# Kernel optimization log

Hardware: AMD Instinct MI355X
Metric: run time of the kernel (lower is better)

## Reference

```python
import jax, jax.numpy as jnp
import numpy as np

EPS = 1e-5


def _ln(t):
    # Custom LayerNorm from the source: unbiased variance (torch.var default),
    # gamma=ones, beta=zeros (plain tensors, never trained) -> plain normalize.
    m = t.mean(axis=-1, keepdims=True)
    v = t.var(axis=-1, keepdims=True, ddof=1)
    return (t - m) / jnp.sqrt(v + EPS)


def setup_inputs() -> dict:
    key = jax.random.key(0)
    B, T, C, H = 4, 2048, 1024, 16
    hs = C // H
    ks = jax.random.split(key, 10)
    s_in = (1.0 / C) ** 0.5   # nn.Linear default init scale (approx, uniform->normal ok for ref)
    s_ff = (1.0 / (4 * C)) ** 0.5
    return {
        "x": jax.random.normal(ks[0], (B, T, C), jnp.float32),
        "Wq": jax.random.normal(ks[1], (H, C, hs), jnp.float32) * s_in,
        "Wk": jax.random.normal(ks[2], (H, C, hs), jnp.float32) * s_in,
        "Wv": jax.random.normal(ks[3], (H, C, hs), jnp.float32) * s_in,
        "Wo": jax.random.normal(ks[4], (C, C), jnp.float32) * s_in,
        "bo": jnp.zeros((C,), jnp.float32),
        "W1": jax.random.normal(ks[5], (C, 4 * C), jnp.float32) * s_in,
        "b1": jnp.zeros((4 * C,), jnp.float32),
        "W2": jax.random.normal(ks[6], (4 * C, C), jnp.float32) * s_ff,
        "b2": jnp.zeros((C,), jnp.float32),
    }


def reference(x, Wq, Wk, Wv, Wo, bo, W1, b1, W2, b2):
    B, T, C = x.shape
    H, _, hs = Wq.shape
    # per-head projections (equivalent to the Python loop over Head modules)
    q = jnp.einsum('btc,hcd->bhtd', x, Wq)
    k = jnp.einsum('btc,hcd->bhtd', x, Wk)
    v = jnp.einsum('btc,hcd->bhtd', x, Wv)
    scores = jnp.einsum('bhtd,bhsd->bhts', q, k) * (hs ** -0.5)
    causal = jnp.tril(jnp.ones((T, T), dtype=bool))
    scores = jnp.where(causal, scores, jnp.float32(-jnp.inf))
    w = jax.nn.softmax(scores, axis=-1)          # dropout is identity in eval
    o = jnp.einsum('bhts,bhsd->bhtd', w, v)
    o = o.transpose(0, 2, 1, 3).reshape(B, T, C)  # concat heads
    attn = o @ Wo + bo
    x1 = x + _ln(attn)
    ff = jax.nn.relu(x1 @ W1 + b1) @ W2 + b2
    return x1 + _ln(ff)
```

## Files before the change

### kernel.cpp

```cpp
#include <hip/hip_runtime.h>
#include <hip/hip_bf16.h>

using bf16 = __hip_bfloat16;
typedef __attribute__((ext_vector_type(8))) short s8v;
typedef __attribute__((ext_vector_type(4))) float f4v;
typedef __attribute__((ext_vector_type(16))) float f16v;
typedef __attribute__((ext_vector_type(4))) unsigned int u4v;

#define QSCALE 0.18033688011112042f

__device__ __forceinline__ void gld_lds16(const void* g, void* l) {
  __builtin_amdgcn_global_load_lds(
      (const __attribute__((address_space(1))) void*)g,
      (__attribute__((address_space(3))) void*)l, 16, 0, 0);
}

__device__ __forceinline__ unsigned short bfbits(float f) {
  bf16 t = __float2bfloat16(f);
  return *reinterpret_cast<unsigned short*>(&t);
}

__device__ __forceinline__ unsigned int pk2(float lo, float hi) {
  return (unsigned int)bfbits(lo) | ((unsigned int)bfbits(hi) << 16);
}

__device__ __forceinline__ void lswap(unsigned int& a, unsigned int& b) {
  asm("v_permlane32_swap_b32 %0, %1" : "+v"(a), "+v"(b));
}

__global__ __launch_bounds__(256) void f32_to_bf16_k(const float* __restrict__ in,
                                                     bf16* __restrict__ out, size_t n) {
  const size_t i = ((size_t)blockIdx.x * 256 + threadIdx.x) * 4;
  if (i + 3 < n) {
    const float4 v = *(const float4*)(in + i);
    out[i + 0] = __float2bfloat16(v.x);
    out[i + 1] = __float2bfloat16(v.y);
    out[i + 2] = __float2bfloat16(v.z);
    out[i + 3] = __float2bfloat16(v.w);
  }
}

__global__ __launch_bounds__(256) void tr_to_bf16_k(const float* __restrict__ in,
                                                    bf16* __restrict__ out,
                                                    int R, int C,
                                                    size_t inb, size_t outb) {
  __shared__ float tile[32][33];
  in  += (size_t)blockIdx.z * inb;
  out += (size_t)blockIdx.z * outb;
  const int r0 = blockIdx.y * 32, c0 = blockIdx.x * 32;
  const int tx = threadIdx.x & 31, ty = threadIdx.x >> 5;
#pragma unroll
  for (int i = 0; i < 4; ++i)
    tile[ty + i * 8][tx] = in[(size_t)(r0 + ty + i * 8) * C + c0 + tx];
  __syncthreads();
#pragma unroll
  for (int i = 0; i < 4; ++i)
    out[(size_t)(c0 + ty + i * 8) * R + r0 + tx] = __float2bfloat16(tile[tx][ty + i * 8]);
}

template <int MODE, int BN>
__global__ __launch_bounds__(512, 2) void gemmT(const bf16* __restrict__ A,
                                                const bf16* __restrict__ B,
                                                const float* __restrict__ bias,
                                                float* __restrict__ Cf,
                                                bf16* __restrict__ Cb,
                                                bf16* __restrict__ Vout,
                                                int M, int N, int K) {
  constexpr int NF = BN / 64;
  constexpr int BH = BN / 128;
  __shared__ __attribute__((aligned(16))) bf16 AS[2][256 * 64];
  __shared__ __attribute__((aligned(16))) bf16 BS[2][BN * 64];

  const int tid  = threadIdx.x;
  const int wid  = tid >> 6;
  const int lane = tid & 63;
  const int l16  = lane & 15;
  const int quad = lane >> 4;
  const int wm   = wid >> 2;
  const int wn   = wid & 3;

  const int gx  = gridDim.x;
  const int nwg = gx * gridDim.y;
  int lin = blockIdx.y * gx + blockIdx.x;
  lin = (lin & 7) * (nwg >> 3) + (lin >> 3);
  const int bm = (lin / gx) * 256;
  const int bn = (lin % gx) * BN;

  const int sr   = tid >> 3;
  const int scol = ((tid & 7) ^ (sr & 7)) << 3;
  const bf16* Asrc = A + (size_t)(bm + sr) * K + scol;
  const bf16* Bsrc = B + (size_t)(bn + sr) * K + scol;
  char* const AW0 = (char*)&AS[0][0] + wid * 1024;
  char* const AW1 = (char*)&AS[1][0] + wid * 1024;
  char* const BW0 = (char*)&BS[0][0] + wid * 1024;
  char* const BW1 = (char*)&BS[1][0] + wid * 1024;

  const int sq  = (quad ^ (l16 & 7)) << 4;
  const int rdA = l16 * 128 + sq;
  const int rdB = wn * (BN / 4) * 128 + l16 * 128 + sq;

#define STAGE_A2(dst, src) \
  do { gld_lds16((src), (dst)); gld_lds16((src) + (size_t)64 * K, (dst) + 8192); } while (0)
#define STAGE_BH(dst, src) \
  do { gld_lds16((src), (dst)); \
       if constexpr (BH == 2) gld_lds16((src) + (size_t)64 * K, (dst) + 8192); } while (0)
#define WAIT_B_INFLIGHT() \
  do { if constexpr (BN == 256) asm volatile("s_waitcnt vmcnt(4)" ::: "memory"); \
       else                     asm volatile("s_waitcnt vmcnt(2)" ::: "memory"); } while (0)

  f4v acc[8][NF];
#pragma unroll
  for (int i = 0; i < 8; ++i)
#pragma unroll
    for (int j = 0; j < NF; ++j) acc[i][j] = (f4v){0.f, 0.f, 0.f, 0.f};

  const int NT = K >> 6;

  STAGE_A2(AW0,         Asrc);
  STAGE_A2(AW0 + 16384, Asrc + (size_t)128 * K);
  STAGE_BH(BW0,             Bsrc);
  STAGE_BH(BW0 + BH * 8192, Bsrc + (size_t)(BH * 64) * K);
  STAGE_BH(BW1,             Bsrc + 64);
  STAGE_BH(BW1 + BH * 8192, Bsrc + (size_t)(BH * 64) * K + 64);
  WAIT_B_INFLIGHT();
  asm volatile("s_barrier" ::: "memory");

  s8v bfrag[NF][2];
  for (int u = 0; u < NT; ++u) {
    const int bsel = u & 1;
    const char* AsB = (const char*)&AS[bsel][0];
    const char* BsB = (const char*)&BS[bsel][0];
    char* const AWn = bsel ? AW0 : AW1;
    char* const BWc = bsel ? BW1 : BW0;
    const bf16* An = Asrc + (size_t)(u + 1) * 64;
    const bf16* Bn = Bsrc + (size_t)(u + 2) * 64;
#pragma unroll
    for (int p = 0; p < 4; ++p) {
      s8v afrag[2][2];
#pragma unroll
      for (int j = 0; j < 2; ++j)
#pragma unroll
        for (int kk = 0; kk < 2; ++kk)
          afrag[j][kk] = *(const s8v*)(AsB +
              ((wm * 16384 + (p * 2 + j) * 2048 + rdA) ^ (kk << 6)));
      if (p == 0) {
#pragma unroll
        for (int nf = 0; nf < NF; ++nf)
#pragma unroll
          for (int kk = 0; kk < 2; ++kk)
            bfrag[nf][kk] = *(const s8v*)(BsB + ((nf * 2048 + rdB) ^ (kk << 6)));
      }
      if (p == 0 && u + 1 < NT) STAGE_A2(AWn,         An);
      if (p == 1 && u + 1 < NT) STAGE_A2(AWn + 16384, An + (size_t)128 * K);
      if (p == 2 && u + 2 < NT) STAGE_BH(BWc,             Bn);
      if (p == 3 && u + 2 < NT) STAGE_BH(BWc + BH * 8192, Bn + (size_t)(BH * 64) * K);
      asm volatile("s_barrier" ::: "memory");
      asm volatile("s_waitcnt lgkmcnt(0)" ::: "memory");
      __builtin_amdgcn_sched_barrier(0);
      __builtin_amdgcn_s_setprio(1);
#pragma unroll
      for (int kk = 0; kk < 2; ++kk)
#pragma unroll
        for (int j = 0; j < 2; ++j)
#pragma unroll
          for (int nf = 0; nf < NF; ++nf)
            acc[p * 2 + j][nf] = __builtin_amdgcn_mfma_f32_16x16x32_bf16(
                afrag[j][kk], bfrag[nf][kk], acc[p * 2 + j][nf], 0, 0, 0);
      __builtin_amdgcn_s_setprio(0);
      if (p == 3) {
        if (u + 2 < NT) WAIT_B_INFLIGHT();
        else            asm volatile("s_waitcnt vmcnt(0)" ::: "memory");
      }
      asm volatile("s_barrier" ::: "memory");
    }
  }
#undef STAGE_A2
#undef STAGE_BH
#undef WAIT_B_INFLIGHT

  const size_t ldc = (size_t)N;
#pragma unroll
  for (int mf = 0; mf < 8; ++mf) {
#pragma unroll
    for (int nf = 0; nf < NF; ++nf) {
      const int col  = bn + wn * (BN / 4) + nf * 16 + l16;
      const int row0 = bm + wm * 128 + mf * 16 + quad * 4;
      if (MODE == 0) {
        if (col < 2048) {
          const float sc = (col < 1024) ? QSCALE : 1.0f;
#pragma unroll
          for (int r = 0; r < 4; ++r)
            Cb[(size_t)(row0 + r) * ldc + col] = __float2bfloat16(acc[mf][nf][r] * sc);
        } else {
          ushort4 pk;
          pk.x = bfbits(acc[mf][nf][0]);
          pk.y = bfbits(acc[mf][nf][1]);
          pk.z = bfbits(acc[mf][nf][2]);
          pk.w = bfbits(acc[mf][nf][3]);
          const int bb = row0 >> 11, t = row0 & 2047;
          *(ushort4*)&Vout[((size_t)(bb * 1024 + col - 2048)) * 2048 + t] = pk;
        }
      } else {
        const float bv = bias[col];
#pragma unroll
        for (int r = 0; r < 4; ++r) {
          const float v = acc[mf][nf][r] + bv;
          if (MODE == 1) Cf[(size_t)(row0 + r) * ldc + col] = v;
          else           Cb[(size_t)(row0 + r) * ldc + col] = __float2bfloat16(fmaxf(v, 0.f));
        }
      }
    }
  }
}

__global__ __launch_bounds__(256, 3) void attn_mfma(const bf16* __restrict__ qkv,
                                                    const bf16* __restrict__ vtg,
                                                    bf16* __restrict__ o) {
  __shared__ __attribute__((aligned(16))) bf16 KsS[2][64 * 64];
  __shared__ __attribute__((aligned(16))) bf16 VtS[2][64 * 64];
  __shared__ __attribute__((aligned(16))) float tS[128];

  const int tid  = threadIdx.x;
  const int w    = tid >> 6;
  const int lane = tid & 63;
  const int l32  = lane & 31;
  const int hi   = lane >> 5;
  const int xq   = l32 & 7;

  const int lin = blockIdx.x;
  const int q2  = lin >> 8;
  const int rr  = lin & 255;
  const int tq  = rr >> 6;
  const int bh  = rr & 63;
  const int b   = bh & 3;
  const int h   = bh >> 2;
  const int qt  = (q2 == 0) ? (15 - tq)
                : (q2 == 1) ? (8 + tq)
                : (q2 == 2) ? (4 + tq)
                            : (3 - tq);

  const bf16* qbase = qkv + (size_t)b * 2048 * 3072 + h * 64;
  const bf16* kbase = qbase + 1024;
  const bf16* vbase = vtg + (size_t)(b * 1024 + h * 64) * 2048;

  const int rsub = lane >> 3;
  const int sseg = (lane & 7) ^ rsub;
  const int d0 = (w * 16) * 64;
  const int d1 = (w * 16 + 8) * 64;

  const int nkt = 2 * qt + 2;
  const int qmin_w = qt * 128 + w * 32;
  const int qmax_w = qmin_w + 31;
  const int q_lane = qmin_w + l32;

  s8v qf[4];
#pragma unroll
  for (int ks = 0; ks < 4; ++ks)
    qf[ks] = *(const s8v*)(qbase + (size_t)q_lane * 3072 + ks * 16 + hi * 8);

  float m_run = -1.0e38f, l_run = 0.f;
  f16v oacc[2];
#pragma unroll
  for (int dn = 0; dn < 2; ++dn)
#pragma unroll
    for (int r = 0; r < 16; ++r) oacc[dn][r] = 0.f;

  const bf16* kg = kbase + (size_t)(w * 16 + rsub) * 3072 + sseg * 8;
  const bf16* vg = vbase + (size_t)(w * 16 + rsub) * 2048 + sseg * 8;

  gld_lds16(kg,                    &KsS[0][d0]);
  gld_lds16(kg + (size_t)8 * 3072, &KsS[0][d1]);
  gld_lds16(vg,                    &VtS[0][d0]);
  gld_lds16(vg + (size_t)8 * 2048, &VtS[0][d1]);
  kg += (size_t)64 * 3072; vg += 64;

  for (int kt = 0; kt < nkt; ++kt) {
    const int cb = kt & 1;

    if (kt + 1 < nkt) {
      const int nb = cb ^ 1;
      gld_lds16(kg,                    &KsS[nb][d0]);
      gld_lds16(kg + (size_t)8 * 3072, &KsS[nb][d1]);
      gld_lds16(vg,                    &VtS[nb][d0]);
      gld_lds16(vg + (size_t)8 * 2048, &VtS[nb][d1]);
      kg += (size_t)64 * 3072; vg += 64;
      asm volatile("s_waitcnt vmcnt(4)" ::: "memory");
    } else {
      asm volatile("s_waitcnt vmcnt(0)" ::: "memory");
    }
    asm volatile("s_barrier" ::: "memory");

    {
      const int kmmax = min(1, (qmax_w - kt * 64) >> 5);
      const bool diag = (kt * 64 + 63 > qmin_w);

      f16v sacc[2];
#pragma unroll
      for (int km = 0; km < 2; ++km)
#pragma unroll
        for (int r = 0; r < 16; ++r) sacc[km][r] = 0.f;

      for (int km = 0; km <= kmmax; ++km)
#pragma unroll
        for (int ks = 0; ks < 4; ++ks) {
          const s8v kf = *(const s8v*)&KsS[cb][(km * 32 + l32) * 64 +
                                               (((2 * ks + hi) ^ xq) << 3)];
          sacc[km] = __builtin_amdgcn_mfma_f32_32x32x16_bf16(kf, qf[ks], sacc[km], 0, 0, 0);
        }

      if (diag) {
        for (int km = 0; km <= kmmax; ++km)
#pragma unroll
          for (int r = 0; r < 16; ++r) {
            const int key = kt * 64 + km * 32 + (r & 3) + 8 * (r >> 2) + 4 * hi;
            if (key > q_lane) sacc[km][r] = -3.0e38f;
          }
      }

      float pmax = -3.0e38f;
#pragma unroll
      for (int km = 0; km < 2; ++km)
        if (km <= kmmax)
#pragma unroll
          for (int r = 0; r < 16; ++r) pmax = fmaxf(pmax, sacc[km][r]);
      pmax = fmaxf(pmax, __shfl_xor(pmax, 32));

      float mref = m_run;
      if (!__all(pmax <= m_run + 8.f)) {
        const float mnew = fmaxf(m_run, pmax);
        const float alpha = __builtin_amdgcn_exp2f(m_run - mnew);
        m_run = mnew; mref = mnew;
        l_run *= alpha;
        tS[w * 32 + l32] = alpha;
        f4v aF[4];
#pragma unroll
        for (int g2 = 0; g2 < 4; ++g2)
          aF[g2] = *(const f4v*)&tS[w * 32 + g2 * 8 + hi * 4];
#pragma unroll
        for (int dn = 0; dn < 2; ++dn)
#pragma unroll
          for (int r = 0; r < 16; ++r) oacc[dn][r] *= aF[r >> 2][r & 3];
      }

      float rs = 0.f;
      s8v pfr[4];
#pragma unroll
      for (int km = 0; km < 2; ++km)
        if (km <= kmmax) {
          float pv[16];
#pragma unroll
          for (int r = 0; r < 16; ++r) {
            pv[r] = __builtin_amdgcn_exp2f(sacc[km][r] - mref);
            rs += pv[r];
          }
          unsigned int u0 = pk2(pv[0], pv[1]),  u1 = pk2(pv[2], pv[3]);
          unsigned int u2 = pk2(pv[4], pv[5]),  u3 = pk2(pv[6], pv[7]);
          lswap(u0, u2); lswap(u1, u3);
          u4v f0 = (u4v){u0, u1, u2, u3};
          pfr[2 * km] = *(s8v*)&f0;
          unsigned int v0 = pk2(pv[8], pv[9]),   v1 = pk2(pv[10], pv[11]);
          unsigned int v2 = pk2(pv[12], pv[13]), v3 = pk2(pv[14], pv[15]);
          lswap(v0, v2); lswap(v1, v3);
          u4v f1 = (u4v){v0, v1, v2, v3};
          pfr[2 * km + 1] = *(s8v*)&f1;
        }
      rs += __shfl_xor(rs, 32);
      l_run += rs;

#pragma unroll
      for (int ks = 0; ks < 4; ++ks)
        if ((ks >> 1) <= kmmax) {
#pragma unroll
          for (int dn = 0; dn < 2; ++dn) {
            const s8v vf = *(const s8v*)&VtS[cb][(dn * 32 + l32) * 64 +
                                                 (((2 * ks + hi) ^ xq) << 3)];
            oacc[dn] = __builtin_amdgcn_mfma_f32_32x32x16_bf16(pfr[ks], vf, oacc[dn], 0, 0, 0);
          }
        }
    }
    asm volatile("s_barrier" ::: "memory");
  }

  tS[w * 32 + l32] = l_run;
  f4v lF[4];
#pragma unroll
  for (int g2 = 0; g2 < 4; ++g2)
    lF[g2] = *(const f4v*)&tS[w * 32 + g2 * 8 + hi * 4];

#pragma unroll
  for (int r = 0; r < 16; ++r) {
    const float inv = __builtin_amdgcn_rcpf(lF[r >> 2][r & 3]);
    const int row = qt * 128 + w * 32 + (r & 3) + 8 * (r >> 2) + 4 * hi;
    bf16* dst = o + ((size_t)b * 2048 + row) * 1024 + h * 64 + l32;
    dst[0]  = __float2bfloat16(oacc[0][r] * inv);
    dst[32] = __float2bfloat16(oacc[1][r] * inv);
  }
}

__global__ __launch_bounds__(256) void ln_res(const float* __restrict__ xres,
                                              const float* __restrict__ t,
                                              float* __restrict__ xo,
                                              bf16* __restrict__ xob) {
  __shared__ float red[2][4];
  const int tid = threadIdx.x;
  const size_t base = (size_t)blockIdx.x * 1024;
  float v[4];
  float s = 0.f;
#pragma unroll
  for (int i = 0; i < 4; ++i) { v[i] = t[base + tid + i * 256]; s += v[i]; }
#pragma unroll
  for (int off = 32; off > 0; off >>= 1) s += __shfl_xor(s, off, 64);
  if ((tid & 63) == 0) red[0][tid >> 6] = s;
  __syncthreads();
  const float mean = (red[0][0] + red[0][1] + red[0][2] + red[0][3]) * (1.f / 1024.f);
  float ss = 0.f;
#pragma unroll
  for (int i = 0; i < 4; ++i) { const float d = v[i] - mean; ss += d * d; }
#pragma unroll
  for (int off = 32; off > 0; off >>= 1) ss += __shfl_xor(ss, off, 64);
  if ((tid & 63) == 0) red[1][tid >> 6] = ss;
  __syncthreads();
  const float var = (red[1][0] + red[1][1] + red[1][2] + red[1][3]) * (1.f / 1023.f);
  const float rstd = rsqrtf(var + 1e-5f);
#pragma unroll
  for (int i = 0; i < 4; ++i) {
    const size_t idx = base + tid + i * 256;
    const float r = xres[idx] + (v[i] - mean) * rstd;
    xo[idx] = r;
    if (xob) xob[idx] = __float2bfloat16(r);
  }
}

extern "C" void kernel_launch(void* const* d_in, const int* in_sizes, int n_in,
                              void* d_out, int out_size, void* d_ws, size_t ws_size,
                              hipStream_t stream) {
  const float* x  = (const float*)d_in[0];
  const float* Wq = (const float*)d_in[1];
  const float* Wk = (const float*)d_in[2];
  const float* Wv = (const float*)d_in[3];
  const float* Wo = (const float*)d_in[4];
  const float* bo = (const float*)d_in[5];
  const float* W1 = (const float*)d_in[6];
  const float* b1 = (const float*)d_in[7];
  const float* W2 = (const float*)d_in[8];
  const float* b2 = (const float*)d_in[9];
  float* out = (float*)d_out;

  char* ws = (char*)d_ws;
  bf16* qkv_bf = (bf16*)(ws);
  bf16* x_bf   = (bf16*)(ws + 50331648);
  bf16* WqkvT  = (bf16*)(ws + 67108864);
  bf16* WoT    = (bf16*)(ws + 73400320);
  bf16* W1T    = (bf16*)(ws + 75497472);
  bf16* W2T    = (bf16*)(ws + 83886080);
  bf16* o_bf   = (bf16*)(ws + 92274688);
  float* attn  = (float*)(ws + 109051904);
  float* x1    = (float*)(ws + 142606336);
  bf16* x1b    = (bf16*)(ws + 176160768);
  bf16* vt     = (bf16*)(ws + 192937984);
  bf16* h1     = (bf16*)(ws);
  float* ff    = (float*)(ws + 109051904);

  f32_to_bf16_k<<<8192, 256, 0, stream>>>(x, x_bf, (size_t)8388608);
  tr_to_bf16_k<<<dim3(2, 32, 16), 256, 0, stream>>>(Wq, WqkvT,               1024, 64,   65536, 65536);
  tr_to_bf16_k<<<dim3(2, 32, 16), 256, 0, stream>>>(Wk, WqkvT + 1024 * 1024, 1024, 64,   65536, 65536);
  tr_to_bf16_k<<<dim3(2, 32, 16), 256, 0, stream>>>(Wv, WqkvT + 2048 * 1024, 1024, 64,   65536, 65536);
  tr_to_bf16_k<<<dim3(32, 32, 1), 256, 0, stream>>>(Wo, WoT,                 1024, 1024, 0, 0);
  tr_to_bf16_k<<<dim3(128, 32, 1), 256, 0, stream>>>(W1, W1T,                1024, 4096, 0, 0);
  tr_to_bf16_k<<<dim3(32, 128, 1), 256, 0, stream>>>(W2, W2T,                4096, 1024, 0, 0);

  gemmT<0, 256><<<dim3(12, 32), 512, 0, stream>>>(x_bf, WqkvT, nullptr, nullptr, qkv_bf, vt, 8192, 3072, 1024);

  attn_mfma<<<1024, 256, 0, stream>>>(qkv_bf, vt, o_bf);

  gemmT<1, 128><<<dim3(8, 32), 512, 0, stream>>>(o_bf, WoT, bo, attn, nullptr, nullptr, 8192, 1024, 1024);

  ln_res<<<8192, 256, 0, stream>>>(x, attn, x1, x1b);

  gemmT<2, 256><<<dim3(16, 32), 512, 0, stream>>>(x1b, W1T, b1, nullptr, h1, nullptr, 8192, 4096, 1024);

  gemmT<1, 128><<<dim3(8, 32), 512, 0, stream>>>(h1, W2T, b2, ff, nullptr, nullptr, 8192, 1024, 4096);

  ln_res<<<8192, 256, 0, stream>>>(x1, ff, out, nullptr);
}
```

Before: 509.6 us.

## Restructure GEMM phases for narrow tiles and tighten attention inner loop

For GEMM variants with BN != 256, the K-step is split into two phases of four A-row fragments instead of four phases of two, which halves the barriers per step and groups the staging loads. In the attention kernel, warps skip fully masked key tiles, the first MFMA takes a zero accumulator so the explicit zeroing is gone, and the max and sum reductions become trees to shorten dependency chains. s_setprio is raised around the MFMA blocks to favour matrix issue. Bigger phases raise register pressure, and the tree reductions change float summation order slightly.

After: 484.3 us. 1.05x faster.

```diff
diff --git a/kernel.cpp b/kernel.cpp
--- a/kernel.cpp
+++ b/kernel.cpp
@@ -134,44 +134,91 @@
     char* const BWc = bsel ? BW1 : BW0;
     const bf16* An = Asrc + (size_t)(u + 1) * 64;
     const bf16* Bn = Bsrc + (size_t)(u + 2) * 64;
-#pragma unroll
-    for (int p = 0; p < 4; ++p) {
-      s8v afrag[2][2];
-#pragma unroll
-      for (int j = 0; j < 2; ++j)
+
+    if constexpr (BN == 256) {
+#pragma unroll
+      for (int p = 0; p < 4; ++p) {
+        s8v afrag[2][2];
+#pragma unroll
+        for (int j = 0; j < 2; ++j)
+#pragma unroll
+          for (int kk = 0; kk < 2; ++kk)
+            afrag[j][kk] = *(const s8v*)(AsB +
+                ((wm * 16384 + (p * 2 + j) * 2048 + rdA) ^ (kk << 6)));
+        if (p == 0) {
+#pragma unroll
+          for (int nf = 0; nf < NF; ++nf)
+#pragma unroll
+            for (int kk = 0; kk < 2; ++kk)
+              bfrag[nf][kk] = *(const s8v*)(BsB + ((nf * 2048 + rdB) ^ (kk << 6)));
+        }
+        if (p == 0 && u + 1 < NT) STAGE_A2(AWn,         An);
+        if (p == 1 && u + 1 < NT) STAGE_A2(AWn + 16384, An + (size_t)128 * K);
+        if (p == 2 && u + 2 < NT) STAGE_BH(BWc,             Bn);
+        if (p == 3 && u + 2 < NT) STAGE_BH(BWc + BH * 8192, Bn + (size_t)(BH * 64) * K);
+        asm volatile("s_barrier" ::: "memory");
+        asm volatile("s_waitcnt lgkmcnt(0)" ::: "memory");
+        __builtin_amdgcn_sched_barrier(0);
+        __builtin_amdgcn_s_setprio(1);
 #pragma unroll
         for (int kk = 0; kk < 2; ++kk)
-          afrag[j][kk] = *(const s8v*)(AsB +
-              ((wm * 16384 + (p * 2 + j) * 2048 + rdA) ^ (kk << 6)));
-      if (p == 0) {
-#pragma unroll
-        for (int nf = 0; nf < NF; ++nf)
+#pragma unroll
+          for (int j = 0; j < 2; ++j)
+#pragma unroll
+            for (int nf = 0; nf < NF; ++nf)
+              acc[p * 2 + j][nf] = __builtin_amdgcn_mfma_f32_16x16x32_bf16(
+                  afrag[j][kk], bfrag[nf][kk], acc[p * 2 + j][nf], 0, 0, 0);
+        __builtin_amdgcn_s_setprio(0);
+        if (p == 3) {
+          if (u + 2 < NT) WAIT_B_INFLIGHT();
+          else            asm volatile("s_waitcnt vmcnt(0)" ::: "memory");
+        }
+        asm volatile("s_barrier" ::: "memory");
+      }
+    } else {
+#pragma unroll
+      for (int p2 = 0; p2 < 2; ++p2) {
+        s8v afrag[4][2];
+#pragma unroll
+        for (int j = 0; j < 4; ++j)
 #pragma unroll
           for (int kk = 0; kk < 2; ++kk)
-            bfrag[nf][kk] = *(const s8v*)(BsB + ((nf * 2048 + rdB) ^ (kk << 6)));
-      }
-      if (p == 0 && u + 1 < NT) STAGE_A2(AWn,         An);
-      if (p == 1 && u + 1 < NT) STAGE_A2(AWn + 16384, An + (size_t)128 * K);
-      if (p == 2 && u + 2 < NT) STAGE_BH(BWc,             Bn);
-      if (p == 3 && u + 2 < NT) STAGE_BH(BWc + BH * 8192, Bn + (size_t)(BH * 64) * K);
-      asm volatile("s_barrier" ::: "memory");
-      asm volatile("s_waitcnt lgkmcnt(0)" ::: "memory");
-      __builtin_amdgcn_sched_barrier(0);
-      __builtin_amdgcn_s_setprio(1);
-#pragma unroll
-      for (int kk = 0; kk < 2; ++kk)
-#pragma unroll
-        for (int j = 0; j < 2; ++j)
+            afrag[j][kk] = *(const s8v*)(AsB +
+                ((wm * 16384 + (p2 * 4 + j) * 2048 + rdA) ^ (kk << 6)));
+        if (p2 == 0) {
 #pragma unroll
           for (int nf = 0; nf < NF; ++nf)
-            acc[p * 2 + j][nf] = __builtin_amdgcn_mfma_f32_16x16x32_bf16(
-                afrag[j][kk], bfrag[nf][kk], acc[p * 2 + j][nf], 0, 0, 0);
-      __builtin_amdgcn_s_setprio(0);
-      if (p == 3) {
-        if (u + 2 < NT) WAIT_B_INFLIGHT();
-        else            asm volatile("s_waitcnt vmcnt(0)" ::: "memory");
-      }
-      asm volatile("s_barrier" ::: "memory");
+#pragma unroll
+            for (int kk = 0; kk < 2; ++kk)
+              bfrag[nf][kk] = *(const s8v*)(BsB + ((nf * 2048 + rdB) ^ (kk << 6)));
+        }
+        if (p2 == 0 && u + 1 < NT) {
+          STAGE_A2(AWn,         An);
+          STAGE_A2(AWn + 16384, An + (size_t)128 * K);
+        }
+        if (p2 == 1 && u + 2 < NT) {
+          STAGE_BH(BWc,             Bn);
+          STAGE_BH(BWc + BH * 8192, Bn + (size_t)(BH * 64) * K);
+        }
+        asm volatile("s_barrier" ::: "memory");
+        asm volatile("s_waitcnt lgkmcnt(0)" ::: "memory");
+        __builtin_amdgcn_sched_barrier(0);
+        __builtin_amdgcn_s_setprio(1);
+#pragma unroll
+        for (int kk = 0; kk < 2; ++kk)
+#pragma unroll
+          for (int j = 0; j < 4; ++j)
+#pragma unroll
+            for (int nf = 0; nf < NF; ++nf)
+              acc[p2 * 4 + j][nf] = __builtin_amdgcn_mfma_f32_16x16x32_bf16(
+                  afrag[j][kk], bfrag[nf][kk], acc[p2 * 4 + j][nf], 0, 0, 0);
+        __builtin_amdgcn_s_setprio(0);
+        if (p2 == 1) {
+          if (u + 2 < NT) WAIT_B_INFLIGHT();
+          else            asm volatile("s_waitcnt vmcnt(0)" ::: "memory");
+        }
+        asm volatile("s_barrier" ::: "memory");
+      }
     }
   }
 #undef STAGE_A2
@@ -264,6 +311,10 @@
   for (int dn = 0; dn < 2; ++dn)
 #pragma unroll
     for (int r = 0; r < 16; ++r) oacc[dn][r] = 0.f;
+
+  f16v z16;
+#pragma unroll
+  for (int r = 0; r < 16; ++r) z16[r] = 0.f;
 
   const bf16* kg = kbase + (size_t)(w * 16 + rsub) * 3072 + sseg * 8;
   const bf16* vg = vbase + (size_t)(w * 16 + rsub) * 2048 + sseg * 8;
@@ -290,23 +341,26 @@
     }
     asm volatile("s_barrier" ::: "memory");
 
-    {
+    if (kt * 64 <= qmax_w) {
       const int kmmax = min(1, (qmax_w - kt * 64) >> 5);
       const bool diag = (kt * 64 + 63 > qmin_w);
 
       f16v sacc[2];
-#pragma unroll
-      for (int km = 0; km < 2; ++km)
-#pragma unroll
-        for (int r = 0; r < 16; ++r) sacc[km][r] = 0.f;
-
-      for (int km = 0; km <= kmmax; ++km)
-#pragma unroll
-        for (int ks = 0; ks < 4; ++ks) {
+      __builtin_amdgcn_s_setprio(1);
+      for (int km = 0; km <= kmmax; ++km) {
+        {
+          const s8v kf = *(const s8v*)&KsS[cb][(km * 32 + l32) * 64 +
+                                               ((hi ^ xq) << 3)];
+          sacc[km] = __builtin_amdgcn_mfma_f32_32x32x16_bf16(kf, qf[0], z16, 0, 0, 0);
+        }
+#pragma unroll
+        for (int ks = 1; ks < 4; ++ks) {
           const s8v kf = *(const s8v*)&KsS[cb][(km * 32 + l32) * 64 +
                                                (((2 * ks + hi) ^ xq) << 3)];
           sacc[km] = __builtin_amdgcn_mfma_f32_32x32x16_bf16(kf, qf[ks], sacc[km], 0, 0, 0);
         }
+      }
+      __builtin_amdgcn_s_setprio(0);
 
       if (diag) {
         for (int km = 0; km <= kmmax; ++km)
@@ -317,12 +371,21 @@
           }
       }
 
-      float pmax = -3.0e38f;
-#pragma unroll
-      for (int km = 0; km < 2; ++km)
-        if (km <= kmmax)
-#pragma unroll
-          for (int r = 0; r < 16; ++r) pmax = fmaxf(pmax, sacc[km][r]);
+      float pmax;
+      {
+        float a[8];
+#pragma unroll
+        for (int i = 0; i < 8; ++i)
+          a[i] = fmaxf(sacc[0][2 * i], sacc[0][2 * i + 1]);
+        if (kmmax) {
+#pragma unroll
+          for (int i = 0; i < 8; ++i)
+            a[i] = fmaxf(a[i], fmaxf(sacc[1][2 * i], sacc[1][2 * i + 1]));
+        }
+        const float b0 = fmaxf(fmaxf(a[0], a[1]), fmaxf(a[2], a[3]));
+        const float b1 = fmaxf(fmaxf(a[4], a[5]), fmaxf(a[6], a[7]));
+        pmax = fmaxf(b0, b1);
+      }
       pmax = fmaxf(pmax, __shfl_xor(pmax, 32));
 
       float mref = m_run;
@@ -349,10 +412,13 @@
         if (km <= kmmax) {
           float pv[16];
 #pragma unroll
-          for (int r = 0; r < 16; ++r) {
+          for (int r = 0; r < 16; ++r)
             pv[r] = __builtin_amdgcn_exp2f(sacc[km][r] - mref);
-            rs += pv[r];
-          }
+          const float s0 = (pv[0] + pv[1]) + (pv[2] + pv[3]);
+          const float s1 = (pv[4] + pv[5]) + (pv[6] + pv[7]);
+          const float s2 = (pv[8] + pv[9]) + (pv[10] + pv[11]);
+          const float s3 = (pv[12] + pv[13]) + (pv[14] + pv[15]);
+          rs += (s0 + s1) + (s2 + s3);
           unsigned int u0 = pk2(pv[0], pv[1]),  u1 = pk2(pv[2], pv[3]);
           unsigned int u2 = pk2(pv[4], pv[5]),  u3 = pk2(pv[6], pv[7]);
           lswap(u0, u2); lswap(u1, u3);
@@ -367,6 +433,7 @@
       rs += __shfl_xor(rs, 32);
       l_run += rs;
 
+      __builtin_amdgcn_s_setprio(1);
 #pragma unroll
       for (int ks = 0; ks < 4; ++ks)
         if ((ks >> 1) <= kmmax) {
@@ -377,6 +444,7 @@
             oacc[dn] = __builtin_amdgcn_mfma_f32_32x32x16_bf16(pfr[ks], vf, oacc[dn], 0, 0, 0);
           }
         }
+      __builtin_amdgcn_s_setprio(0);
     }
     asm volatile("s_barrier" ::: "memory");
   }
```
